# Performance work log

Hardware: AMD Instinct MI355X
Metric: run time of the kernel (lower is better)

Reference implementation:

```python
import jax, jax.numpy as jnp
import numpy as np

NV, NF, DIM = 6144, 12288, 256


def _linear(x, W, b):
    # torch nn.Linear: x @ W.T + b, W has shape (out, in)
    return x @ W.T + b


def _agg(X, A, Wf, bf, Wg, bg):
    # AGG: out_fc = Linear(A @ X); out_gagg = Linear(A @ out_fc)  (eval mode: dropout is identity)
    out_fc = _linear(A @ X, Wf, bf)
    out_g = _linear(A @ out_fc, Wg, bg)
    return jax.nn.relu(out_fc + out_g)


def setup_inputs() -> dict:
    key = jax.random.key(0)
    ks = jax.random.split(key, 18)
    primal = jax.random.normal(ks[0], (NV, DIM), jnp.float32)
    # degree-normalized adjacency (docstring): scale uniform entries by 1/N for stable row sums
    A_primal = jax.random.uniform(ks[1], (NV, NV), jnp.float32) * (1.0 / NV)
    A_dual = jax.random.uniform(ks[2], (NF, NF), jnp.float32) * (1.0 / NF)
    A = jax.random.uniform(ks[3], (NV, NF), jnp.float32) * (1.0 / NF)
    faces = jax.random.randint(ks[4], (NF, 3), 0, NV)

    w = lambda k, shp: jax.random.normal(k, shp, jnp.float32) * 0.05
    return {
        "primal": primal, "A_primal": A_primal, "A_dual": A_dual, "A": A, "faces": faces,
        # 3 primal AGG layers (fc + gagg), stacked on leading axis
        "pW": w(ks[5], (3, DIM, DIM)), "pb": w(ks[6], (3, DIM)),
        "pgW": w(ks[7], (3, DIM, DIM)), "pgb": w(ks[8], (3, DIM)),
        # 3 dual AGG layers
        "dW": w(ks[9], (3, DIM, DIM)), "db": w(ks[10], (3, DIM)),
        "dgW": w(ks[11], (3, DIM, DIM)), "dgb": w(ks[12], (3, DIM)),
        # PDF linears: (dim, 2*dim)
        "Wp": w(ks[13], (DIM, 2 * DIM)), "bp": w(ks[14], (DIM,)),
        "Wd": w(ks[15], (DIM, 2 * DIM)), "bd": w(ks[16], (DIM,)),
    }


def reference(primal, A_primal, A_dual, A, faces, pW, pb, pgW, pgb, dW, db, dgW, dgb, Wp, bp, Wd, bd):
    x_p = primal
    x_d = (1.0 / 3.0) * (A.T @ primal)  # primal_dual
    primal_outs, dual_outs = [], []
    for i in range(3):
        primal_outs.append(x_p)
        x_p = _agg(x_p, A_primal, pW[i], pb[i], pgW[i], pgb[i]) + x_p
    for i in range(3):
        dual_outs.append(x_d)
        x_d = _agg(x_d, A_dual, dW[i], db[i], dgW[i], dgb[i]) + x_d
    # PDF: DAP gather-reduce  (N_f, 3, dim) -> (N_f, dim)
    f = jnp.mean(jnp.abs(x_p[faces] - x_d[:, None, :]), axis=1)
    out_dual = jax.nn.relu(_linear(jnp.concatenate([x_d, f], axis=1), Wd, bd))
    mapped = A @ f  # dual_primal
    out_primal = jax.nn.relu(_linear(jnp.concatenate([x_p, mapped], axis=1), Wp, bp))
    return (out_primal + x_p, out_dual + x_d, *primal_outs, *dual_outs)
```

## Files before the change

kernel.cpp:

```cpp
#include <hip/hip_runtime.h>


typedef short short8 __attribute__((ext_vector_type(8)));
typedef float floatx4 __attribute__((ext_vector_type(4)));
typedef unsigned short ushort4v __attribute__((ext_vector_type(4)));
typedef unsigned short u16;

#define DIMN 256
#define GBM 128
#define GBN 256
#define GBK 64

static const int kNV = 6144;
static const int kNF = 12288;
static const int SLAB = 768;

__device__ __forceinline__ float bf2f(u16 u) {
  union { unsigned int i; float f; } x; x.i = ((unsigned int)u) << 16; return x.f;
}
__device__ __forceinline__ u16 f2bf(float f) {
  union { float f; unsigned int i; } x; x.f = f;
  unsigned int r = x.i + 0x7fffu + ((x.i >> 16) & 1u);
  return (u16)(r >> 16);
}
__device__ __forceinline__ void gld_lds16(const void* g, void* l) {
  __builtin_amdgcn_global_load_lds((__attribute__((address_space(1))) void*)(g),
                                   (__attribute__((address_space(3))) void*)(l),
                                   16, 0, 0);
}

__global__ __launch_bounds__(512, 1)
void gemm_bf16_k(const void* __restrict__ A0, int A0is32,
                 const void* __restrict__ A1, int A1is32, int K1,
                 int lda0, int lda1,
                 const void* __restrict__ Bt, int Btis32, int ldb,
                 void* __restrict__ P, int M, int kchunk, int pbf16,
                 int fused, const float* __restrict__ bias,
                 const u16* __restrict__ addmat, int do_relu,
                 const float* __restrict__ resid,
                 float* __restrict__ outf, u16* __restrict__ out16)
{
  __shared__ __align__(16) u16 As[2][GBM * GBK];
  __shared__ __align__(16) u16 Bs[2][GBN * GBK];

  const int m0 = blockIdx.x * GBM;
  const int kb = blockIdx.z * kchunk;
  const int nkt = kchunk / GBK;

  const int tid = threadIdx.x;
  const int wid = tid >> 6;
  const int lane = tid & 63;
  const int wr = wid >> 2;
  const int wc = wid & 3;
  const int srow = lane >> 3;
  const int skk = (lane & 7) << 3;

  floatx4 acc[4][4];
  floatx4 zz = {0.f, 0.f, 0.f, 0.f};
#pragma unroll
  for (int i = 0; i < 4; ++i)
#pragma unroll
    for (int j = 0; j < 4; ++j) acc[i][j] = zz;

  auto stage = [&](int buf, int k0) {
    const void* base; int lda, is32, kl;
    if (k0 < K1) { base = A0; lda = lda0; is32 = A0is32; kl = k0; }
    else         { base = A1; lda = lda1; is32 = A1is32; kl = k0 - K1; }
    if (is32) {
      const float* F = (const float*)base;
#pragma unroll
      for (int j = 0; j < 2; ++j) {
        int c = (wid << 1) + j;
        const float* src = F + (size_t)(m0 + (c << 3) + srow) * lda + kl + skk;
        floatx4 f0 = *(const floatx4*)src;
        floatx4 f1 = *(const floatx4*)(src + 4);
        short8 v;
#pragma unroll
        for (int e = 0; e < 4; ++e) { v[e] = (short)f2bf(f0[e]); v[4 + e] = (short)f2bf(f1[e]); }
        *(short8*)&As[buf][(c << 9) + (lane << 3)] = v;
      }
    } else {
      const u16* U = (const u16*)base;
#pragma unroll
      for (int j = 0; j < 2; ++j) {
        int c = (wid << 1) + j;
        gld_lds16(U + (size_t)(m0 + (c << 3) + srow) * lda + kl + skk,
                  (void*)&As[buf][c << 9]);
      }
    }
    if (Btis32) {
      const float* F = (const float*)Bt;
#pragma unroll
      for (int j = 0; j < 4; ++j) {
        int c = (wid << 2) + j;
        const float* src = F + (size_t)((c << 3) + srow) * ldb + k0 + skk;
        floatx4 f0 = *(const floatx4*)src;
        floatx4 f1 = *(const floatx4*)(src + 4);
        short8 v;
#pragma unroll
        for (int e = 0; e < 4; ++e) { v[e] = (short)f2bf(f0[e]); v[4 + e] = (short)f2bf(f1[e]); }
        *(short8*)&Bs[buf][(c << 9) + (lane << 3)] = v;
      }
    } else {
      const u16* U = (const u16*)Bt;
#pragma unroll
      for (int j = 0; j < 4; ++j) {
        int c = (wid << 2) + j;
        gld_lds16(U + (size_t)((c << 3) + srow) * ldb + k0 + skk,
                  (void*)&Bs[buf][c << 9]);
      }
    }
  };

  int cur = 0;
  stage(0, kb);
  for (int kt = 0; kt < nkt; ++kt) {
    __syncthreads();
    if (kt + 1 < nkt) stage(cur ^ 1, kb + (kt + 1) * GBK);
#pragma unroll
    for (int ks = 0; ks < 2; ++ks) {
      short8 a[4], b[4];
      const int ko = (ks << 5) + ((lane >> 4) << 3);
#pragma unroll
      for (int mi = 0; mi < 4; ++mi)
        a[mi] = *(const short8*)&As[cur][((wr << 6) + (mi << 4) + (lane & 15)) * GBK + ko];
#pragma unroll
      for (int ni = 0; ni < 4; ++ni)
        b[ni] = *(const short8*)&Bs[cur][((wc << 6) + (ni << 4) + (lane & 15)) * GBK + ko];
#pragma unroll
      for (int mi = 0; mi < 4; ++mi)
#pragma unroll
        for (int ni = 0; ni < 4; ++ni)
          acc[mi][ni] = __builtin_amdgcn_mfma_f32_16x16x32_bf16(a[mi], b[ni], acc[mi][ni], 0, 0, 0);
    }
    cur ^= 1;
  }

  if (fused) {
#pragma unroll
    for (int mi = 0; mi < 4; ++mi) {
#pragma unroll
      for (int ni = 0; ni < 4; ++ni) {
        const int mb = m0 + (wr << 6) + (mi << 4) + ((lane >> 4) << 2);
        const int n = (wc << 6) + (ni << 4) + (lane & 15);
        const float bv = bias ? bias[n] : 0.f;
#pragma unroll
        for (int r = 0; r < 4; ++r) {
          const size_t idx = (size_t)(mb + r) * DIMN + n;
          float t = acc[mi][ni][r] + bv;
          if (addmat) t += bf2f(addmat[idx]);
          if (do_relu) t = fmaxf(t, 0.f);
          if (resid) t += resid[idx];
          if (outf) outf[idx] = t;
          if (out16) out16[idx] = f2bf(t);
        }
      }
    }
  } else if (pbf16) {
    u16* Pz = (u16*)P + (size_t)blockIdx.z * (size_t)M * DIMN;
#pragma unroll
    for (int mi = 0; mi < 4; ++mi) {
#pragma unroll
      for (int ni = 0; ni < 4; ++ni) {
        const int mb = m0 + (wr << 6) + (mi << 4) + ((lane >> 4) << 2);
        const int n = (wc << 6) + (ni << 4) + (lane & 15);
#pragma unroll
        for (int r = 0; r < 4; ++r)
          Pz[(size_t)(mb + r) * DIMN + n] = f2bf(acc[mi][ni][r]);
      }
    }
  } else {
    float* Pz = (float*)P + (size_t)blockIdx.z * (size_t)M * DIMN;
#pragma unroll
    for (int mi = 0; mi < 4; ++mi) {
#pragma unroll
      for (int ni = 0; ni < 4; ++ni) {
        const int mb = m0 + (wr << 6) + (mi << 4) + ((lane >> 4) << 2);
        const int n = (wc << 6) + (ni << 4) + (lane & 15);
#pragma unroll
        for (int r = 0; r < 4; ++r)
          Pz[(size_t)(mb + r) * DIMN + n] = acc[mi][ni][r];
      }
    }
  }
}

__global__ __launch_bounds__(256)
void finalize_k(const void* __restrict__ P, int pbf16, int S, int Mrows, float scale,
                const float* __restrict__ bias, const u16* __restrict__ addmat,
                int do_relu, const float* __restrict__ resid,
                float* __restrict__ out, u16* __restrict__ out16)
{
  const size_t MN = (size_t)Mrows * DIMN;
  const size_t i4 = (((size_t)blockIdx.x * blockDim.x) + threadIdx.x) * 4;
  if (i4 >= MN) return;
  floatx4 v = {0.f, 0.f, 0.f, 0.f};
  if (pbf16) {
    const u16* Pu = (const u16*)P;
    for (int s = 0; s < S; ++s) {
      ushort4v p4 = *(const ushort4v*)(Pu + (size_t)s * MN + i4);
#pragma unroll
      for (int j = 0; j < 4; ++j) v[j] += bf2f(p4[j]);
    }
  } else {
    const float* Pf = (const float*)P;
    for (int s = 0; s < S; ++s) v += *(const floatx4*)(Pf + (size_t)s * MN + i4);
  }
  const int n = (int)(i4 & 255);
  floatx4 bf = {0.f,0.f,0.f,0.f}, af = {0.f,0.f,0.f,0.f}, rf = {0.f,0.f,0.f,0.f};
  if (bias) bf = *(const floatx4*)(bias + n);
  if (addmat) {
#pragma unroll
    for (int j = 0; j < 4; ++j) af[j] = bf2f(addmat[i4 + j]);
  }
  if (resid) rf = *(const floatx4*)(resid + i4);
  floatx4 o;
#pragma unroll
  for (int j = 0; j < 4; ++j) {
    float t = v[j] * scale + bf[j] + af[j];
    if (do_relu) t = fmaxf(t, 0.f);
    o[j] = t + rf[j];
  }
  if (out) *(floatx4*)(out + i4) = o;
  if (out16) {
    unsigned long long q = 0;
#pragma unroll
    for (int j = 0; j < 4; ++j) q |= ((unsigned long long)f2bf(o[j])) << (16 * j);
    *(unsigned long long*)(out16 + i4) = q;
  }
}

__global__ __launch_bounds__(256)
void transpose_k(const void* __restrict__ in, int is32, int ldin,
                 u16* __restrict__ out, int ldout)
{
  __shared__ __align__(16) u16 t[64][64];
  const int c0 = blockIdx.x << 6;
  const int r0 = blockIdx.y << 6;
  const int tid = threadIdx.x;
  const int lr = tid >> 3;
  const int lc = (tid & 7) << 3;
#pragma unroll
  for (int h = 0; h < 2; ++h) {
    const int r = lr + (h << 5);
    short8 v;
    if (is32) {
      const float* F = (const float*)in;
      const float* src = F + (size_t)(r0 + r) * ldin + (c0 + lc);
      floatx4 f0 = *(const floatx4*)src;
      floatx4 f1 = *(const floatx4*)(src + 4);
#pragma unroll
      for (int e = 0; e < 4; ++e) { v[e] = (short)f2bf(f0[e]); v[4 + e] = (short)f2bf(f1[e]); }
    } else {
      v = *(const short8*)((const u16*)in + (size_t)(r0 + r) * ldin + (c0 + lc));
    }
    *(short8*)&t[r][lc ^ ((r >> 3) << 3)] = v;
  }
  __syncthreads();
#pragma unroll
  for (int h = 0; h < 2; ++h) {
    const int oc = lr + (h << 5);
    short8 v;
#pragma unroll
    for (int e = 0; e < 8; ++e)
      v[e] = (short)t[lc + e][oc ^ ((lc >> 3) << 3)];
    *(short8*)&out[(size_t)(c0 + oc) * ldout + (r0 + lc)] = v;
  }
}

__global__ __launch_bounds__(256)
void cvt8_k(const float* __restrict__ in, u16* __restrict__ out, size_t n)
{
  const size_t i = (((size_t)blockIdx.x << 8) + threadIdx.x) << 3;
  if (i >= n) return;
  floatx4 f0 = *(const floatx4*)(in + i);
  floatx4 f1 = *(const floatx4*)(in + i + 4);
  short8 v;
#pragma unroll
  for (int e = 0; e < 4; ++e) { v[e] = (short)f2bf(f0[e]); v[4 + e] = (short)f2bf(f1[e]); }
  *(short8*)(out + i) = v;
}

__global__ __launch_bounds__(256)
void face_gather_k(const float* __restrict__ xp, const float* __restrict__ xd,
                   const int* __restrict__ faces, u16* __restrict__ f)
{
  const int fi = blockIdx.x;
  const int j = threadIdx.x;
  const int a = faces[fi * 3 + 0];
  const int b = faces[fi * 3 + 1];
  const int c = faces[fi * 3 + 2];
  const float xv = xd[(size_t)fi * DIMN + j];
  const float s = fabsf(xp[(size_t)a * DIMN + j] - xv)
                + fabsf(xp[(size_t)b * DIMN + j] - xv)
                + fabsf(xp[(size_t)c * DIMN + j] - xv);
  f[(size_t)fi * DIMN + j] = f2bf(s * (1.0f / 3.0f));
}

extern "C" void kernel_launch(void* const* d_in, const int* in_sizes, int n_in,
                              void* d_out, int out_size, void* d_ws, size_t ws_size,
                              hipStream_t stream)
{
  (void)in_sizes; (void)n_in; (void)out_size;
  const float* primal   = (const float*)d_in[0];
  const float* A_primal = (const float*)d_in[1];
  const float* A_dual   = (const float*)d_in[2];
  const float* A        = (const float*)d_in[3];
  const int* faces      = (const int*)d_in[4];
  const float* pW  = (const float*)d_in[5];
  const float* pb  = (const float*)d_in[6];
  const float* pgW = (const float*)d_in[7];
  const float* pgb = (const float*)d_in[8];
  const float* dW  = (const float*)d_in[9];
  const float* db  = (const float*)d_in[10];
  const float* dgW = (const float*)d_in[11];
  const float* dgb = (const float*)d_in[12];
  const float* Wp  = (const float*)d_in[13];
  const float* bp  = (const float*)d_in[14];
  const float* Wd  = (const float*)d_in[15];
  const float* bd  = (const float*)d_in[16];

  char* wsp = (char*)d_ws;
  auto alloc = [&](size_t bytes) -> void* {
    void* p = (void*)wsp;
    wsp += (bytes + 255) & ~(size_t)255;
    return p;
  };
  const size_t NVD = (size_t)kNV * DIMN, NFD = (size_t)kNF * DIMN;
  u16* XT    = (u16*)alloc(NFD * 2);
  u16* TB    = (u16*)alloc((size_t)SLAB * kNV * 2);
  u16* t1    = (u16*)alloc(NFD * 2);
  u16* fc    = (u16*)alloc(NFD * 2);
  void* P    = alloc((size_t)8 * NFD * 4);
  const size_t bigElems = (size_t)kNF * kNF + (size_t)kNF * kNV + (size_t)kNV * kNV;
  const size_t need = (size_t)(wsp - (char*)d_ws) + bigElems * 2 + 4096;
  const bool big = ws_size >= need;
  u16 *Ad16 = nullptr, *At16 = nullptr, *Ap16 = nullptr;
  if (big) {
    Ad16 = (u16*)alloc((size_t)kNF * kNF * 2);
    At16 = (u16*)alloc((size_t)kNF * kNV * 2);
    Ap16 = (u16*)alloc((size_t)kNV * kNV * 2);
  }

  float* out0  = (float*)d_out;
  float* out1  = out0 + NVD;
  float* pouts = out1 + NFD;
  float* douts = pouts + 3 * NVD;

  auto gemmP = [&](const void* A0p, int a0is32, int lda0,
                   const void* Btp, int ldb, int M, int K, int S) {
    gemm_bf16_k<<<dim3(M / GBM, 1, S), dim3(512), 0, stream>>>(
        A0p, a0is32, nullptr, 0, K, lda0, 0, Btp, 0, ldb, P, M, K / S, 1,
        0, nullptr, nullptr, 0, nullptr, nullptr, nullptr);
  };
  auto gemmF = [&](const void* A0p, int a0is32, int lda0,
                   const void* A1p, int a1is32, int lda1, int K1,
                   const float* Btp, int ldb, int M, int K,
                   const float* bias, const u16* add, int relu,
                   const float* resid, float* outf, u16* out16) {
    gemm_bf16_k<<<dim3(M / GBM, 1, 1), dim3(512), 0, stream>>>(
        A0p, a0is32, A1p, a1is32, K1, lda0, lda1, Btp, 1, ldb, P, M, K, 0,
        1, bias, add, relu, resid, outf, out16);
  };
  auto fin = [&](int M, int S, float scale, float* out, u16* out16) {
    finalize_k<<<dim3((unsigned)((size_t)M * DIMN / 1024)), dim3(256), 0, stream>>>(
        P, 1, S, M, scale, nullptr, nullptr, 0, nullptr, out, out16);
  };
  auto tranp = [&](const void* in, int is32, int ldin, u16* out, int ldout,
                   int R, int C) {
    transpose_k<<<dim3(C / 64, R / 64), dim3(256), 0, stream>>>(
        in, is32, ldin, out, ldout);
  };
  auto cvt = [&](const float* in, u16* out, size_t n) {
    cvt8_k<<<dim3((unsigned)(n / 2048)), dim3(256), 0, stream>>>(in, out, n);
  };

  const void *AdP, *ApP;
  int cf;
  if (big) {
    cvt(A_dual, Ad16, (size_t)kNF * kNF);
    cvt(A_primal, Ap16, (size_t)kNV * kNV);
    tranp(A, 1, kNF, At16, kNV, kNV, kNF);
    AdP = Ad16; ApP = Ap16; cf = 0;
  } else {
    AdP = A_dual; ApP = A_primal; cf = 1;
  }

  tranp(primal, 1, DIMN, XT, kNV, kNV, DIMN);
  hipMemcpyAsync(pouts, primal, NVD * 4, hipMemcpyDeviceToDevice, stream);

  if (big) {
    gemmP(At16, 0, kNV, XT, kNV, kNF, kNV, 8);
    fin(kNF, 8, 1.0f / 3.0f, douts, nullptr);
  } else {
    for (int s = 0; s < kNF / SLAB; ++s) {
      const int m0 = s * SLAB;
      tranp(A + m0, 1, kNF, TB, kNV, kNV, SLAB);
      gemmP(TB, 0, kNV, XT, kNV, SLAB, kNV, 16);
      fin(SLAB, 16, 1.0f / 3.0f, douts + (size_t)m0 * DIMN, nullptr);
    }
  }

  const float* xpc = primal;
  for (int i = 0; i < 3; ++i) {
    gemmP(ApP, cf, kNV, XT, kNV, kNV, kNV, 16);
    fin(kNV, 16, 1.f, nullptr, t1);
    gemmF(t1, 0, 256, nullptr, 0, 0, 256, pW + (size_t)i * 65536, 256,
          kNV, 256, pb + i * 256, nullptr, 0, nullptr, nullptr, fc);
    tranp(fc, 0, DIMN, TB, kNV, kNV, DIMN);
    gemmP(ApP, cf, kNV, TB, kNV, kNV, kNV, 16);
    fin(kNV, 16, 1.f, nullptr, t1);
    float* nxt = (i < 2) ? (pouts + (size_t)(i + 1) * NVD) : out0;
    gemmF(t1, 0, 256, nullptr, 0, 0, 256, pgW + (size_t)i * 65536, 256,
          kNV, 256, pgb + i * 256, fc, 1, xpc, nxt, nullptr);
    xpc = nxt;
    if (i < 2) tranp(xpc, 1, DIMN, XT, kNV, kNV, DIMN);
  }

  const float* xdc = douts;
  tranp(xdc, 1, DIMN, XT, kNF, kNF, DIMN);
  for (int i = 0; i < 3; ++i) {
    gemmP(AdP, cf, kNF, XT, kNF, kNF, kNF, 8);
    fin(kNF, 8, 1.f, nullptr, t1);
    gemmF(t1, 0, 256, nullptr, 0, 0, 256, dW + (size_t)i * 65536, 256,
          kNF, 256, db + i * 256, nullptr, 0, nullptr, nullptr, fc);
    tranp(fc, 0, DIMN, TB, kNF, kNF, DIMN);
    gemmP(AdP, cf, kNF, TB, kNF, kNF, kNF, 8);
    fin(kNF, 8, 1.f, nullptr, t1);
    float* nxt = (i < 2) ? (douts + (size_t)(i + 1) * NFD) : out1;
    gemmF(t1, 0, 256, nullptr, 0, 0, 256, dgW + (size_t)i * 65536, 256,
          kNF, 256, dgb + i * 256, fc, 1, xdc, nxt, nullptr);
    xdc = nxt;
    if (i < 2) tranp(xdc, 1, DIMN, XT, kNF, kNF, DIMN);
  }

  face_gather_k<<<dim3(kNF), dim3(256), 0, stream>>>(xpc, xdc, faces, t1);
  tranp(t1, 0, DIMN, TB, kNF, kNF, DIMN);
  gemmF(xdc, 1, 256, t1, 0, 256, 256, Wd, 512, kNF, 512,
        bd, nullptr, 1, xdc, out1, nullptr);
  gemmP(A, 1, kNF, TB, kNF, kNV, kNF, 16);
  fin(kNV, 16, 1.f, nullptr, fc);
  gemmF(xpc, 1, 256, fc, 0, 256, 256, Wp, 512, kNV, 512,
        bp, nullptr, 1, xpc, out0, nullptr);
}
```

Baseline: 2.128 ms.

## Split GEMM N across blocks, fuse fp32-to-bf16 adjacency conversion into first GEMM

The GEMM kernel now uses 256-thread blocks computing 128x128 tiles, with the N dimension split across two blocks through a flattened 1D grid, and targets two blocks per CU. The separate conversion kernels for A_primal and A_dual are removed: the first layer's GEMM reads the fp32 matrix, converts it in registers, and writes the bf16 copy for later layers, saving one full pass over the large adjacency matrices. Split-K factors are halved to cut partial-sum traffic and finalize work, and unused fp32 partial and finalize paths are dropped. The first GEMM becomes slower because of fp32 loads and the extra store, and each block now reloads the A tile once per N half.

```diff
diff --git a/kernel.cpp b/kernel.cpp
--- a/kernel.cpp
+++ b/kernel.cpp
@@ -7,8 +7,6 @@
 typedef unsigned short u16;
 
 #define DIMN 256
-#define GBM 128
-#define GBN 256
 #define GBK 64
 
 static const int kNV = 6144;
@@ -29,29 +27,33 @@
                                    16, 0, 0);
 }
 
-__global__ __launch_bounds__(512, 1)
+__global__ __launch_bounds__(256, 2)
 void gemm_bf16_k(const void* __restrict__ A0, int A0is32,
                  const void* __restrict__ A1, int A1is32, int K1,
-                 int lda0, int lda1,
+                 int lda0, int lda1, u16* __restrict__ cvtw,
                  const void* __restrict__ Bt, int Btis32, int ldb,
-                 void* __restrict__ P, int M, int kchunk, int pbf16,
+                 void* __restrict__ P, int M, int nx, int kchunk,
                  int fused, const float* __restrict__ bias,
                  const u16* __restrict__ addmat, int do_relu,
                  const float* __restrict__ resid,
                  float* __restrict__ outf, u16* __restrict__ out16)
 {
-  __shared__ __align__(16) u16 As[2][GBM * GBK];
-  __shared__ __align__(16) u16 Bs[2][GBN * GBK];
-
-  const int m0 = blockIdx.x * GBM;
-  const int kb = blockIdx.z * kchunk;
+  __shared__ __align__(16) u16 As[2][128 * GBK];
+  __shared__ __align__(16) u16 Bs[2][128 * GBK];
+
+  const int d = blockIdx.x;
+  const int y = d & 1;
+  const int bx = (d >> 1) % nx;
+  const int bz = (d >> 1) / nx;
+  const int m0 = bx << 7;
+  const int n0 = y << 7;
+  const int kb = bz * kchunk;
   const int nkt = kchunk / GBK;
 
   const int tid = threadIdx.x;
   const int wid = tid >> 6;
   const int lane = tid & 63;
-  const int wr = wid >> 2;
-  const int wc = wid & 3;
+  const int wr = wid >> 1, wc = wid & 1;
   const int srow = lane >> 3;
   const int skk = (lane & 7) << 3;
 
@@ -69,21 +71,22 @@
     if (is32) {
       const float* F = (const float*)base;
 #pragma unroll
-      for (int j = 0; j < 2; ++j) {
-        int c = (wid << 1) + j;
-        const float* src = F + (size_t)(m0 + (c << 3) + srow) * lda + kl + skk;
-        floatx4 f0 = *(const floatx4*)src;
-        floatx4 f1 = *(const floatx4*)(src + 4);
+      for (int j = 0; j < 4; ++j) {
+        int c = (wid << 2) + j;
+        const size_t gi = (size_t)(m0 + (c << 3) + srow) * lda + kl + skk;
+        floatx4 f0 = *(const floatx4*)((const float*)F + gi);
+        floatx4 f1 = *(const floatx4*)((const float*)F + gi + 4);
         short8 v;
 #pragma unroll
         for (int e = 0; e < 4; ++e) { v[e] = (short)f2bf(f0[e]); v[4 + e] = (short)f2bf(f1[e]); }
         *(short8*)&As[buf][(c << 9) + (lane << 3)] = v;
+        if (cvtw && y == 0) *(short8*)(cvtw + gi) = v;
       }
     } else {
       const u16* U = (const u16*)base;
 #pragma unroll
-      for (int j = 0; j < 2; ++j) {
-        int c = (wid << 1) + j;
+      for (int j = 0; j < 4; ++j) {
+        int c = (wid << 2) + j;
         gld_lds16(U + (size_t)(m0 + (c << 3) + srow) * lda + kl + skk,
                   (void*)&As[buf][c << 9]);
       }
@@ -93,9 +96,9 @@
 #pragma unroll
       for (int j = 0; j < 4; ++j) {
         int c = (wid << 2) + j;
-        const float* src = F + (size_t)((c << 3) + srow) * ldb + k0 + skk;
-        floatx4 f0 = *(const floatx4*)src;
-        floatx4 f1 = *(const floatx4*)(src + 4);
+        const size_t gi = (size_t)(n0 + (c << 3) + srow) * ldb + k0 + skk;
+        floatx4 f0 = *(const floatx4*)((const float*)F + gi);
+        floatx4 f1 = *(const floatx4*)((const float*)F + gi + 4);
         short8 v;
 #pragma unroll
         for (int e = 0; e < 4; ++e) { v[e] = (short)f2bf(f0[e]); v[4 + e] = (short)f2bf(f1[e]); }
@@ -106,7 +109,7 @@
 #pragma unroll
       for (int j = 0; j < 4; ++j) {
         int c = (wid << 2) + j;
-        gld_lds16(U + (size_t)((c << 3) + srow) * ldb + k0 + skk,
+        gld_lds16(U + (size_t)(n0 + (c << 3) + srow) * ldb + k0 + skk,
                   (void*)&Bs[buf][c << 9]);
       }
     }
@@ -142,7 +145,7 @@
 #pragma unroll
       for (int ni = 0; ni < 4; ++ni) {
         const int mb = m0 + (wr << 6) + (mi << 4) + ((lane >> 4) << 2);
-        const int n = (wc << 6) + (ni << 4) + (lane & 15);
+        const int n = n0 + (wc << 6) + (ni << 4) + (lane & 15);
         const float bv = bias ? bias[n] : 0.f;
 #pragma unroll
         for (int r = 0; r < 4; ++r) {
@@ -156,71 +159,38 @@
         }
       }
     }
-  } else if (pbf16) {
-    u16* Pz = (u16*)P + (size_t)blockIdx.z * (size_t)M * DIMN;
+  } else {
+    u16* Pz = (u16*)P + (size_t)bz * (size_t)M * DIMN;
 #pragma unroll
     for (int mi = 0; mi < 4; ++mi) {
 #pragma unroll
       for (int ni = 0; ni < 4; ++ni) {
         const int mb = m0 + (wr << 6) + (mi << 4) + ((lane >> 4) << 2);
-        const int n = (wc << 6) + (ni << 4) + (lane & 15);
+        const int n = n0 + (wc << 6) + (ni << 4) + (lane & 15);
 #pragma unroll
         for (int r = 0; r < 4; ++r)
           Pz[(size_t)(mb + r) * DIMN + n] = f2bf(acc[mi][ni][r]);
       }
     }
-  } else {
-    float* Pz = (float*)P + (size_t)blockIdx.z * (size_t)M * DIMN;
-#pragma unroll
-    for (int mi = 0; mi < 4; ++mi) {
-#pragma unroll
-      for (int ni = 0; ni < 4; ++ni) {
-        const int mb = m0 + (wr << 6) + (mi << 4) + ((lane >> 4) << 2);
-        const int n = (wc << 6) + (ni << 4) + (lane & 15);
-#pragma unroll
-        for (int r = 0; r < 4; ++r)
-          Pz[(size_t)(mb + r) * DIMN + n] = acc[mi][ni][r];
-      }
-    }
   }
 }
 
 __global__ __launch_bounds__(256)
-void finalize_k(const void* __restrict__ P, int pbf16, int S, int Mrows, float scale,
-                const float* __restrict__ bias, const u16* __restrict__ addmat,
-                int do_relu, const float* __restrict__ resid,
+void finalize_k(const u16* __restrict__ P, int S, int Mrows, float scale,
                 float* __restrict__ out, u16* __restrict__ out16)
 {
   const size_t MN = (size_t)Mrows * DIMN;
   const size_t i4 = (((size_t)blockIdx.x * blockDim.x) + threadIdx.x) * 4;
   if (i4 >= MN) return;
   floatx4 v = {0.f, 0.f, 0.f, 0.f};
-  if (pbf16) {
-    const u16* Pu = (const u16*)P;
-    for (int s = 0; s < S; ++s) {
-      ushort4v p4 = *(const ushort4v*)(Pu + (size_t)s * MN + i4);
-#pragma unroll
-      for (int j = 0; j < 4; ++j) v[j] += bf2f(p4[j]);
-    }
-  } else {
-    const float* Pf = (const float*)P;
-    for (int s = 0; s < S; ++s) v += *(const floatx4*)(Pf + (size_t)s * MN + i4);
-  }
-  const int n = (int)(i4 & 255);
-  floatx4 bf = {0.f,0.f,0.f,0.f}, af = {0.f,0.f,0.f,0.f}, rf = {0.f,0.f,0.f,0.f};
-  if (bias) bf = *(const floatx4*)(bias + n);
-  if (addmat) {
-#pragma unroll
-    for (int j = 0; j < 4; ++j) af[j] = bf2f(addmat[i4 + j]);
-  }
-  if (resid) rf = *(const floatx4*)(resid + i4);
+  for (int s = 0; s < S; ++s) {
+    ushort4v p4 = *(const ushort4v*)(P + (size_t)s * MN + i4);
+#pragma unroll
+    for (int j = 0; j < 4; ++j) v[j] += bf2f(p4[j]);
+  }
   floatx4 o;
 #pragma unroll
-  for (int j = 0; j < 4; ++j) {
-    float t = v[j] * scale + bf[j] + af[j];
-    if (do_relu) t = fmaxf(t, 0.f);
-    o[j] = t + rf[j];
-  }
+  for (int j = 0; j < 4; ++j) o[j] = v[j] * scale;
   if (out) *(floatx4*)(out + i4) = o;
   if (out16) {
     unsigned long long q = 0;
@@ -266,19 +236,6 @@
       v[e] = (short)t[lc + e][oc ^ ((lc >> 3) << 3)];
     *(short8*)&out[(size_t)(c0 + oc) * ldout + (r0 + lc)] = v;
   }
-}
-
-__global__ __launch_bounds__(256)
-void cvt8_k(const float* __restrict__ in, u16* __restrict__ out, size_t n)
-{
-  const size_t i = (((size_t)blockIdx.x << 8) + threadIdx.x) << 3;
-  if (i >= n) return;
-  floatx4 f0 = *(const floatx4*)(in + i);
-  floatx4 f1 = *(const floatx4*)(in + i + 4);
-  short8 v;
-#pragma unroll
-  for (int e = 0; e < 4; ++e) { v[e] = (short)f2bf(f0[e]); v[4 + e] = (short)f2bf(f1[e]); }
-  *(short8*)(out + i) = v;
 }
 
 __global__ __launch_bounds__(256)
@@ -331,7 +288,7 @@
   u16* TB    = (u16*)alloc((size_t)SLAB * kNV * 2);
   u16* t1    = (u16*)alloc(NFD * 2);
   u16* fc    = (u16*)alloc(NFD * 2);
-  void* P    = alloc((size_t)8 * NFD * 4);
+  u16* P     = (u16*)alloc((size_t)8 * NFD * 2);
   const size_t bigElems = (size_t)kNF * kNF + (size_t)kNF * kNV + (size_t)kNV * kNV;
   const size_t need = (size_t)(wsp - (char*)d_ws) + bigElems * 2 + 4096;
   const bool big = ws_size >= need;
@@ -347,69 +304,63 @@
   float* pouts = out1 + NFD;
   float* douts = pouts + 3 * NVD;
 
-  auto gemmP = [&](const void* A0p, int a0is32, int lda0,
+  auto gemmP = [&](const void* A0p, int a0is32, int lda0, u16* cvtw,
                    const void* Btp, int ldb, int M, int K, int S) {
-    gemm_bf16_k<<<dim3(M / GBM, 1, S), dim3(512), 0, stream>>>(
-        A0p, a0is32, nullptr, 0, K, lda0, 0, Btp, 0, ldb, P, M, K / S, 1,
-        0, nullptr, nullptr, 0, nullptr, nullptr, nullptr);
+    const int nx = M / 128;
+    gemm_bf16_k<<<dim3(nx * 2 * S), dim3(256), 0, stream>>>(
+        A0p, a0is32, nullptr, 0, K, lda0, 0, cvtw, Btp, 0, ldb,
+        P, M, nx, K / S, 0, nullptr, nullptr, 0, nullptr, nullptr, nullptr);
   };
   auto gemmF = [&](const void* A0p, int a0is32, int lda0,
                    const void* A1p, int a1is32, int lda1, int K1,
                    const float* Btp, int ldb, int M, int K,
                    const float* bias, const u16* add, int relu,
                    const float* resid, float* outf, u16* out16) {
-    gemm_bf16_k<<<dim3(M / GBM, 1, 1), dim3(512), 0, stream>>>(
-        A0p, a0is32, A1p, a1is32, K1, lda0, lda1, Btp, 1, ldb, P, M, K, 0,
-        1, bias, add, relu, resid, outf, out16);
+    const int nx = M / 128;
+    gemm_bf16_k<<<dim3(nx * 2), dim3(256), 0, stream>>>(
+        A0p, a0is32, A1p, a1is32, K1, lda0, lda1, nullptr, Btp, 1, ldb,
+        P, M, nx, K, 1, bias, add, relu, resid, outf, out16);
   };
   auto fin = [&](int M, int S, float scale, float* out, u16* out16) {
     finalize_k<<<dim3((unsigned)((size_t)M * DIMN / 1024)), dim3(256), 0, stream>>>(
-        P, 1, S, M, scale, nullptr, nullptr, 0, nullptr, out, out16);
+        P, S, M, scale, out, out16);
   };
   auto tranp = [&](const void* in, int is32, int ldin, u16* out, int ldout,
                    int R, int C) {
     transpose_k<<<dim3(C / 64, R / 64), dim3(256), 0, stream>>>(
         in, is32, ldin, out, ldout);
   };
-  auto cvt = [&](const float* in, u16* out, size_t n) {
-    cvt8_k<<<dim3((unsigned)(n / 2048)), dim3(256), 0, stream>>>(in, out, n);
-  };
-
-  const void *AdP, *ApP;
-  int cf;
-  if (big) {
-    cvt(A_dual, Ad16, (size_t)kNF * kNF);
-    cvt(A_primal, Ap16, (size_t)kNV * kNV);
-    tranp(A, 1, kNF, At16, kNV, kNV, kNF);
-    AdP = Ad16; ApP = Ap16; cf = 0;
-  } else {
-    AdP = A_dual; ApP = A_primal; cf = 1;
-  }
 
   tranp(primal, 1, DIMN, XT, kNV, kNV, DIMN);
   hipMemcpyAsync(pouts, primal, NVD * 4, hipMemcpyDeviceToDevice, stream);
+  if (big) tranp(A, 1, kNF, At16, kNV, kNV, kNF);
 
   if (big) {
-    gemmP(At16, 0, kNV, XT, kNV, kNF, kNV, 8);
-    fin(kNF, 8, 1.0f / 3.0f, douts, nullptr);
+    gemmP(At16, 0, kNV, nullptr, XT, kNV, kNF, kNV, 4);
+    fin(kNF, 4, 1.0f / 3.0f, douts, nullptr);
   } else {
     for (int s = 0; s < kNF / SLAB; ++s) {
       const int m0 = s * SLAB;
       tranp(A + m0, 1, kNF, TB, kNV, kNV, SLAB);
-      gemmP(TB, 0, kNV, XT, kNV, SLAB, kNV, 16);
+      gemmP(TB, 0, kNV, nullptr, XT, kNV, SLAB, kNV, 16);
       fin(SLAB, 16, 1.0f / 3.0f, douts + (size_t)m0 * DIMN, nullptr);
     }
   }
 
   const float* xpc = primal;
   for (int i = 0; i < 3; ++i) {
-    gemmP(ApP, cf, kNV, XT, kNV, kNV, kNV, 16);
-    fin(kNV, 16, 1.f, nullptr, t1);
+    if (big && i == 0)
+      gemmP(A_primal, 1, kNV, Ap16, XT, kNV, kNV, kNV, 8);
+    else
+      gemmP(big ? (const void*)Ap16 : (const void*)A_primal, big ? 0 : 1,
+            kNV, nullptr, XT, kNV, kNV, kNV, 8);
+    fin(kNV, 8, 1.f, nullptr, t1);
     gemmF(t1, 0, 256, nullptr, 0, 0, 256, pW + (size_t)i * 65536, 256,
           kNV, 256, pb + i * 256, nullptr, 0, nullptr, nullptr, fc);
     tranp(fc, 0, DIMN, TB, kNV, kNV, DIMN);
-    gemmP(ApP, cf, kNV, TB, kNV, kNV, kNV, 16);
-    fin(kNV, 16, 1.f, nullptr, t1);
+    gemmP(big ? (const void*)Ap16 : (const void*)A_primal, big ? 0 : 1,
+          kNV, nullptr, TB, kNV, kNV, kNV, 8);
+    fin(kNV, 8, 1.f, nullptr, t1);
     float* nxt = (i < 2) ? (pouts + (size_t)(i + 1) * NVD) : out0;
     gemmF(t1, 0, 256, nullptr, 0, 0, 256, pgW + (size_t)i * 65536, 256,
           kNV, 256, pgb + i * 256, fc, 1, xpc, nxt, nullptr);
@@ -420,13 +371,18 @@
   const float* xdc = douts;
   tranp(xdc, 1, DIMN, XT, kNF, kNF, DIMN);
   for (int i = 0; i < 3; ++i) {
-    gemmP(AdP, cf, kNF, XT, kNF, kNF, kNF, 8);
-    fin(kNF, 8, 1.f, nullptr, t1);
+    if (big && i == 0)
+      gemmP(A_dual, 1, kNF, Ad16, XT, kNF, kNF, kNF, 4);
+    else
+      gemmP(big ? (const void*)Ad16 : (const void*)A_dual, big ? 0 : 1,
+            kNF, nullptr, XT, kNF, kNF, kNF, 4);
+    fin(kNF, 4, 1.f, nullptr, t1);
     gemmF(t1, 0, 256, nullptr, 0, 0, 256, dW + (size_t)i * 65536, 256,
           kNF, 256, db + i * 256, nullptr, 0, nullptr, nullptr, fc);
     tranp(fc, 0, DIMN, TB, kNF, kNF, DIMN);
-    gemmP(AdP, cf, kNF, TB, kNF, kNF, kNF, 8);
-    fin(kNF, 8, 1.f, nullptr, t1);
+    gemmP(big ? (const void*)Ad16 : (const void*)A_dual, big ? 0 : 1,
+          kNF, nullptr, TB, kNF, kNF, kNF, 4);
+    fin(kNF, 4, 1.f, nullptr, t1);
     float* nxt = (i < 2) ? (douts + (size_t)(i + 1) * NFD) : out1;
     gemmF(t1, 0, 256, nullptr, 0, 0, 256, dgW + (size_t)i * 65536, 256,
           kNF, 256, dgb + i * 256, fc, 1, xdc, nxt, nullptr);
@@ -438,8 +394,8 @@
   tranp(t1, 0, DIMN, TB, kNF, kNF, DIMN);
   gemmF(xdc, 1, 256, t1, 0, 256, 256, Wd, 512, kNF, 512,
         bd, nullptr, 1, xdc, out1, nullptr);
-  gemmP(A, 1, kNF, TB, kNF, kNV, kNF, 16);
-  fin(kNV, 16, 1.f, nullptr, fc);
+  gemmP(A, 1, kNF, nullptr, TB, kNF, kNV, kNF, 8);
+  fin(kNV, 8, 1.f, nullptr, fc);
   gemmF(xpc, 1, 256, fc, 0, 256, 256, Wp, 512, kNV, 512,
         bp, nullptr, 1, xpc, out0, nullptr);
 }
```

Result: slower. 2.322 ms (+9.1%).
